# Performance work log

Measured on AMD Instinct MI355X. Metric: run time of the kernel, lower is better.

The kernel has to match this reference:

```python
import jax, jax.numpy as jnp
import numpy as np
import math

HIDDEN = 2048
N_HEADS = 16
HEAD_DIM = HIDDEN // N_HEADS
ROPE_BASE = 10000.0


def setup_inputs() -> dict:
    key = jax.random.key(0)
    ks = jax.random.split(key, 5)
    B, S = 2, 2048
    hidden_states = jax.random.normal(ks[0], (B, S, HIDDEN), dtype=jnp.float32)
    # additive causal mask (bsz, 1, q_len, kv_len)
    causal = jnp.tril(jnp.ones((S, S), dtype=bool))
    attention_mask = jnp.where(causal, 0.0, jnp.finfo(jnp.float32).min)[None, None].astype(jnp.float32)
    attention_mask = jnp.broadcast_to(attention_mask, (B, 1, S, S))
    position_ids = jnp.broadcast_to(jnp.arange(S, dtype=jnp.int32)[None], (B, S))
    scale = 1.0 / math.sqrt(HIDDEN)
    Wq = jax.random.normal(ks[1], (HIDDEN, HIDDEN), dtype=jnp.float32) * scale
    Wk = jax.random.normal(ks[2], (HIDDEN, HIDDEN), dtype=jnp.float32) * scale
    Wv = jax.random.normal(ks[3], (HIDDEN, HIDDEN), dtype=jnp.float32) * scale
    Wo = jax.random.normal(ks[4], (HIDDEN, HIDDEN), dtype=jnp.float32) * scale
    return {"hidden_states": hidden_states, "attention_mask": attention_mask,
            "position_ids": position_ids, "Wq": Wq, "Wk": Wk, "Wv": Wv, "Wo": Wo}


def _rotate_half(x):
    x1, x2 = jnp.split(x, 2, axis=-1)
    return jnp.concatenate([-x2, x1], axis=-1)


def _rope_cos_sin(position_ids, head_dim, dtype):
    inv_freq = 1.0 / (ROPE_BASE ** (jnp.arange(0, head_dim, 2, dtype=jnp.float32) / head_dim))
    freqs = position_ids.astype(jnp.float32)[..., None] * inv_freq  # [B, S, hd/2]
    emb = jnp.concatenate([freqs, freqs], axis=-1)                  # [B, S, hd]
    # unsqueeze head dim -> [B, 1, S, hd]
    return jnp.cos(emb)[:, None].astype(dtype), jnp.sin(emb)[:, None].astype(dtype)


def reference(hidden_states, attention_mask, position_ids, Wq, Wk, Wv, Wo):
    B, S, _ = hidden_states.shape
    H, D = N_HEADS, HEAD_DIM
    # projections (nn.Linear: x @ W.T); split heads -> [B, H, S, D]
    def proj(W):
        return jnp.einsum('bsh,oh->bso', hidden_states, W).reshape(B, S, H, D).transpose(0, 2, 1, 3)
    q, k, v = proj(Wq), proj(Wk), proj(Wv)
    cos, sin = _rope_cos_sin(position_ids, D, hidden_states.dtype)
    q = q * cos + _rotate_half(q) * sin
    k = k * cos + _rotate_half(k) * sin
    scores = jnp.einsum('bhqd,bhkd->bhqk', q, k) / math.sqrt(D)
    scores = scores + attention_mask
    probs = jax.nn.softmax(scores.astype(jnp.float32), axis=-1).astype(q.dtype)
    attn = jnp.einsum('bhqk,bhkd->bhqd', probs, v)
    attn = attn.transpose(0, 2, 1, 3).reshape(B, S, H * D)
    return jnp.einsum('bso,ho->bsh', attn, Wo)
```

## Files before the change

kernel.cpp:

```cpp
#include <hip/hip_runtime.h>
#include <cstdint>

typedef unsigned short u16t;
typedef float v4f __attribute__((ext_vector_type(4)));
typedef short v8s __attribute__((ext_vector_type(8)));

#define HIDDEN 2048
#define NHEAD 16
#define HDIM 128
#define SEQ 2048
#define BATCH 2
#define MROWS (BATCH * SEQ)

__device__ __forceinline__ float bf2f(u16t u) {
  return __builtin_bit_cast(float, (uint32_t)((uint32_t)u << 16));
}
__device__ __forceinline__ u16t f2bf(float f) {
  uint32_t u = __builtin_bit_cast(uint32_t, f);
  u += 0x7FFFu + ((u >> 16) & 1u);
  return (u16t)(u >> 16);
}
__device__ __forceinline__ ushort4 f2bf4(float4 v) {
  ushort4 r;
  r.x = f2bf(v.x); r.y = f2bf(v.y); r.z = f2bf(v.z); r.w = f2bf(v.w);
  return r;
}

__device__ __forceinline__ void gld_lds16(const u16t* g, u16t* l) {
  __builtin_amdgcn_global_load_lds(
      (const __attribute__((address_space(1))) uint32_t*)g,
      (__attribute__((address_space(3))) uint32_t*)l, 16, 0, 0);
}

__global__ __launch_bounds__(256) void cvt_bf16(const float* __restrict__ src,
                                                u16t* __restrict__ dst, int n8) {
  int i = blockIdx.x * 256 + threadIdx.x;
  if (i < n8) {
    float4 a = ((const float4*)src)[2 * i];
    float4 b = ((const float4*)src)[2 * i + 1];
    union { ushort4 h[2]; uint4 u; } pk;
    pk.h[0] = f2bf4(a);
    pk.h[1] = f2bf4(b);
    ((uint4*)dst)[i] = pk.u;
  }
}

__global__ __launch_bounds__(256) void cvt_bf16_w4(
    const float* __restrict__ s0, const float* __restrict__ s1,
    const float* __restrict__ s2, const float* __restrict__ s3,
    u16t* __restrict__ d0, u16t* __restrict__ d1,
    u16t* __restrict__ d2, u16t* __restrict__ d3) {
  int i = blockIdx.x * 256 + threadIdx.x;
  int sel = i >> 19;
  int j = i & 0x7FFFF;
  const float* src = (sel == 0) ? s0 : (sel == 1) ? s1 : (sel == 2) ? s2 : s3;
  u16t* dst = (sel == 0) ? d0 : (sel == 1) ? d1 : (sel == 2) ? d2 : d3;
  float4 a = ((const float4*)src)[2 * j];
  float4 b = ((const float4*)src)[2 * j + 1];
  union { ushort4 h[2]; uint4 u; } pk;
  pk.h[0] = f2bf4(a);
  pk.h[1] = f2bf4(b);
  ((uint4*)dst)[j] = pk.u;
}

template <int OUT>
__global__ __launch_bounds__(512) void gemm8p(const u16t* __restrict__ A,
                                              const u16t* __restrict__ B,
                                              void* __restrict__ Cp) {
  __shared__ u16t lds[73728];

  const int n0 = blockIdx.x * 128;
  const int m0 = blockIdx.y * 256;
  const int t = threadIdx.x;
  const int lane = t & 63;
  const int w = t >> 6;
  const int wm = w >> 2;
  const int wn = w & 3;
  const int l15 = lane & 15;
  const int quad = lane >> 4;
  const int l7 = l15 & 7;

  const int lrow = lane >> 3;
  const int lcol8 = ((lane & 7) ^ lrow) * 8;
  const u16t* Ag = A + (size_t)(m0 + w * 32 + lrow) * HIDDEN + lcol8;
  const u16t* Bg = B + (size_t)(n0 + w * 16 + lrow) * HIDDEN + lcol8;

  const int ca0 = (quad * 8) ^ (l7 * 8);
  const int ca1 = (32 + quad * 8) ^ (l7 * 8);

  v4f acc[8][2];
#pragma unroll
  for (int i = 0; i < 8; ++i)
#pragma unroll
    for (int j = 0; j < 2; ++j) acc[i][j] = (v4f){0.f, 0.f, 0.f, 0.f};

  const int KT = HIDDEN / 64;

#pragma unroll
  for (int tt = 0; tt < 2; ++tt) {
    const int kb = tt * 64;
#pragma unroll
    for (int j = 0; j < 4; ++j)
      gld_lds16(Ag + kb + j * 8 * HIDDEN,
                &lds[tt * 16384 + (w * 4 + j) * 512 + lane * 8]);
#pragma unroll
    for (int j = 0; j < 2; ++j)
      gld_lds16(Bg + kb + j * 8 * HIDDEN,
                &lds[49152 + tt * 8192 + (w * 2 + j) * 512 + lane * 8]);
  }
  asm volatile("s_waitcnt vmcnt(6)" ::: "memory");
  __builtin_amdgcn_s_barrier();

  int b = 0;
  for (int kt = 0; kt < KT; ++kt) {
    const int kb2 = kt * 64 + 128;
    const int b2 = (b >= 1) ? b - 1 : 2;
    const u16t* Asb = &lds[b * 16384];
    const u16t* Bsb = &lds[49152 + b * 8192];
    const bool pre = (kt + 2 < KT);

    v8s b0[2], b1[2];
#pragma unroll
    for (int j = 0; j < 2; ++j) {
      const u16t* p = Bsb + (wn * 32 + j * 16 + l15) * 64;
      b0[j] = *(const v8s*)(p + ca0);
      b1[j] = *(const v8s*)(p + ca1);
    }
    v8s a0[4], a1[4];
#pragma unroll
    for (int i = 0; i < 4; ++i) {
      const u16t* p = Asb + (wm * 128 + i * 16 + l15) * 64;
      a0[i] = *(const v8s*)(p + ca0);
      a1[i] = *(const v8s*)(p + ca1);
    }
    if (pre) {
      gld_lds16(Ag + kb2, &lds[b2 * 16384 + (w * 4 + 0) * 512 + lane * 8]);
      gld_lds16(Ag + kb2 + 8 * HIDDEN, &lds[b2 * 16384 + (w * 4 + 1) * 512 + lane * 8]);
      gld_lds16(Bg + kb2, &lds[49152 + b2 * 8192 + (w * 2 + 0) * 512 + lane * 8]);
    }
    __builtin_amdgcn_s_barrier();
    asm volatile("s_waitcnt lgkmcnt(0)" ::: "memory");
    __builtin_amdgcn_s_setprio(1);
#pragma unroll
    for (int i = 0; i < 4; ++i)
#pragma unroll
      for (int j = 0; j < 2; ++j) {
        acc[i][j] = __builtin_amdgcn_mfma_f32_16x16x32_bf16(a0[i], b0[j], acc[i][j], 0, 0, 0);
        acc[i][j] = __builtin_amdgcn_mfma_f32_16x16x32_bf16(a1[i], b1[j], acc[i][j], 0, 0, 0);
      }
    __builtin_amdgcn_s_setprio(0);
    __builtin_amdgcn_s_barrier();

#pragma unroll
    for (int i = 0; i < 4; ++i) {
      const u16t* p = Asb + (wm * 128 + 64 + i * 16 + l15) * 64;
      a0[i] = *(const v8s*)(p + ca0);
      a1[i] = *(const v8s*)(p + ca1);
    }
    if (pre) {
      gld_lds16(Ag + kb2 + 16 * HIDDEN, &lds[b2 * 16384 + (w * 4 + 2) * 512 + lane * 8]);
      gld_lds16(Ag + kb2 + 24 * HIDDEN, &lds[b2 * 16384 + (w * 4 + 3) * 512 + lane * 8]);
      gld_lds16(Bg + kb2 + 8 * HIDDEN, &lds[49152 + b2 * 8192 + (w * 2 + 1) * 512 + lane * 8]);
    }
    __builtin_amdgcn_s_barrier();
    asm volatile("s_waitcnt lgkmcnt(0)" ::: "memory");
    __builtin_amdgcn_s_setprio(1);
#pragma unroll
    for (int i = 0; i < 4; ++i)
#pragma unroll
      for (int j = 0; j < 2; ++j) {
        acc[4 + i][j] = __builtin_amdgcn_mfma_f32_16x16x32_bf16(a0[i], b0[j], acc[4 + i][j], 0, 0, 0);
        acc[4 + i][j] = __builtin_amdgcn_mfma_f32_16x16x32_bf16(a1[i], b1[j], acc[4 + i][j], 0, 0, 0);
      }
    __builtin_amdgcn_s_setprio(0);
    if (pre) {
      asm volatile("s_waitcnt vmcnt(6)" ::: "memory");
    } else if (kt + 1 < KT) {
      asm volatile("s_waitcnt vmcnt(0)" ::: "memory");
    }
    __builtin_amdgcn_s_barrier();
    b = (b == 2) ? 0 : b + 1;
  }

  if (OUT == 2) {
    u16t* Ct = (u16t*)lds;
    __syncthreads();
#pragma unroll
    for (int i = 0; i < 8; ++i)
#pragma unroll
      for (int j = 0; j < 2; ++j)
#pragma unroll
        for (int r = 0; r < 4; ++r)
          Ct[(wn * 32 + j * 16 + l15) * 264 + wm * 128 + i * 16 + quad * 4 + r] =
              f2bf(acc[i][j][r]);
    __syncthreads();
    u16t* VtOut = (u16t*)Cp;
#pragma unroll
    for (int it = 0; it < 8; ++it) {
      int idx = t + it * 512;
      int nl = idx >> 5;
      int mc = idx & 31;
      *(uint4*)&VtOut[(size_t)(n0 + nl) * MROWS + m0 + mc * 8] =
          *(const uint4*)&Ct[nl * 264 + mc * 8];
    }
  } else {
#pragma unroll
    for (int i = 0; i < 8; ++i) {
#pragma unroll
      for (int j = 0; j < 2; ++j) {
        int col = n0 + wn * 32 + j * 16 + l15;
#pragma unroll
        for (int r = 0; r < 4; ++r) {
          int row = m0 + wm * 128 + i * 16 + quad * 4 + r;
          if (OUT == 1)
            ((float*)Cp)[(size_t)row * HIDDEN + col] = acc[i][j][r];
          else
            ((u16t*)Cp)[(size_t)row * HIDDEN + col] = f2bf(acc[i][j][r]);
        }
      }
    }
  }
}

template <int OUT_F32>
__global__ __launch_bounds__(256) void gemm_a16(const u16t* __restrict__ A,
                                                const void* __restrict__ Bp,
                                                void* __restrict__ Cp) {
  __shared__ u16t As[128 * 32];
  __shared__ u16t Bs[128 * 32];

  const int n0 = blockIdx.x * 128;
  const int m0 = blockIdx.y * 128;
  const int t = threadIdx.x;
  const int lane = t & 63;
  const int w = t >> 6;
  const int wm = w & 1;
  const int wn = w >> 1;
  const int l15 = lane & 15;
  const int quad = lane >> 4;

  v4f acc[4][4];
#pragma unroll
  for (int i = 0; i < 4; ++i)
#pragma unroll
    for (int j = 0; j < 4; ++j) acc[i][j] = (v4f){0.f, 0.f, 0.f, 0.f};

  for (int kb = 0; kb < HIDDEN; kb += 32) {
#pragma unroll
    for (int j = 0; j < 2; ++j) {
      int idx = t + j * 256;
      int row = idx >> 2;
      int ch = (idx & 3) * 8;
      gld_lds16(&A[(size_t)(m0 + row) * HIDDEN + kb + ch], &As[idx * 8]);
    }
    {
      const float* B = (const float*)Bp;
#pragma unroll
      for (int j = 0; j < 4; ++j) {
        int idx = t + j * 256;
        int row = idx >> 3;
        int c4 = (idx & 7) * 4;
        float4 bv = *(const float4*)&B[(size_t)(n0 + row) * HIDDEN + kb + c4];
        *(ushort4*)&Bs[row * 32 + c4] = f2bf4(bv);
      }
    }
    __syncthreads();

    v8s af[4], bf[4];
#pragma unroll
    for (int mt = 0; mt < 4; ++mt)
      af[mt] = *(const v8s*)&As[(wm * 64 + mt * 16 + l15) * 32 + quad * 8];
#pragma unroll
    for (int nt = 0; nt < 4; ++nt)
      bf[nt] = *(const v8s*)&Bs[(wn * 64 + nt * 16 + l15) * 32 + quad * 8];

#pragma unroll
    for (int mt = 0; mt < 4; ++mt)
#pragma unroll
      for (int nt = 0; nt < 4; ++nt)
        acc[mt][nt] = __builtin_amdgcn_mfma_f32_16x16x32_bf16(af[mt], bf[nt], acc[mt][nt], 0, 0, 0);
    __syncthreads();
  }

#pragma unroll
  for (int mt = 0; mt < 4; ++mt) {
#pragma unroll
    for (int nt = 0; nt < 4; ++nt) {
      int col = n0 + wn * 64 + nt * 16 + l15;
#pragma unroll
      for (int r = 0; r < 4; ++r) {
        int row = m0 + wm * 64 + mt * 16 + quad * 4 + r;
        if (OUT_F32)
          ((float*)Cp)[(size_t)row * HIDDEN + col] = acc[mt][nt][r];
        else
          ((u16t*)Cp)[(size_t)row * HIDDEN + col] = f2bf(acc[mt][nt][r]);
      }
    }
  }
}

__global__ __launch_bounds__(256) void gemm_vt_f32(const u16t* __restrict__ A,
                                                   const void* __restrict__ Bp,
                                                   u16t* __restrict__ VtOut) {
  __shared__ u16t As[128 * 32];
  __shared__ u16t Bs[128 * 32];
  __shared__ u16t Ct[128 * 136];

  const int n0 = blockIdx.x * 128;
  const int m0 = blockIdx.y * 128;
  const int t = threadIdx.x;
  const int lane = t & 63;
  const int w = t >> 6;
  const int wm = w & 1;
  const int wn = w >> 1;
  const int l15 = lane & 15;
  const int quad = lane >> 4;

  v4f acc[4][4];
#pragma unroll
  for (int i = 0; i < 4; ++i)
#pragma unroll
    for (int j = 0; j < 4; ++j) acc[i][j] = (v4f){0.f, 0.f, 0.f, 0.f};

  for (int kb = 0; kb < HIDDEN; kb += 32) {
#pragma unroll
    for (int j = 0; j < 2; ++j) {
      int idx = t + j * 256;
      int row = idx >> 2;
      int ch = (idx & 3) * 8;
      gld_lds16(&A[(size_t)(m0 + row) * HIDDEN + kb + ch], &As[idx * 8]);
    }
    {
      const float* B = (const float*)Bp;
#pragma unroll
      for (int j = 0; j < 4; ++j) {
        int idx = t + j * 256;
        int row = idx >> 3;
        int c4 = (idx & 7) * 4;
        float4 bv = *(const float4*)&B[(size_t)(n0 + row) * HIDDEN + kb + c4];
        *(ushort4*)&Bs[row * 32 + c4] = f2bf4(bv);
      }
    }
    __syncthreads();

    v8s af[4], bf[4];
#pragma unroll
    for (int mt = 0; mt < 4; ++mt)
      af[mt] = *(const v8s*)&As[(wm * 64 + mt * 16 + l15) * 32 + quad * 8];
#pragma unroll
    for (int nt = 0; nt < 4; ++nt)
      bf[nt] = *(const v8s*)&Bs[(wn * 64 + nt * 16 + l15) * 32 + quad * 8];

#pragma unroll
    for (int mt = 0; mt < 4; ++mt)
#pragma unroll
      for (int nt = 0; nt < 4; ++nt)
        acc[mt][nt] = __builtin_amdgcn_mfma_f32_16x16x32_bf16(af[mt], bf[nt], acc[mt][nt], 0, 0, 0);
    __syncthreads();
  }

#pragma unroll
  for (int mt = 0; mt < 4; ++mt)
#pragma unroll
    for (int nt = 0; nt < 4; ++nt)
#pragma unroll
      for (int r = 0; r < 4; ++r)
        Ct[(wn * 64 + nt * 16 + l15) * 136 + (wm * 64 + mt * 16 + quad * 4 + r)] =
            f2bf(acc[mt][nt][r]);
  __syncthreads();

#pragma unroll
  for (int j = 0; j < 8; ++j) {
    int idx = t + j * 256;
    int nl = idx >> 4;
    int mc = idx & 15;
    *(uint4*)&VtOut[(size_t)(n0 + nl) * MROWS + m0 + mc * 8] =
        *(const uint4*)&Ct[nl * 136 + mc * 8];
  }
}

__global__ __launch_bounds__(256) void rope_k(u16t* __restrict__ q, u16t* __restrict__ k) {
  int idx = blockIdx.x * 256 + threadIdx.x;
  int i = idx & 63;
  int h = (idx >> 6) & (NHEAD - 1);
  int m = idx >> 10;
  int s = m & (SEQ - 1);
  float inv = __expf(-(float)i * 0.14391156831212787f);
  float th = (float)s * inv;
  float sn, cs;
  __sincosf(th, &sn, &cs);
  size_t base = (size_t)m * HIDDEN + h * HDIM + i;
  {
    float a = bf2f(q[base]), b = bf2f(q[base + 64]);
    q[base] = f2bf(a * cs - b * sn);
    q[base + 64] = f2bf(b * cs + a * sn);
  }
  {
    float a = bf2f(k[base]), b = bf2f(k[base + 64]);
    k[base] = f2bf(a * cs - b * sn);
    k[base + 64] = f2bf(b * cs + a * sn);
  }
}

__global__ __launch_bounds__(512) void flash2(const u16t* __restrict__ Q,
                                              const u16t* __restrict__ K,
                                              const u16t* __restrict__ Vt,
                                              u16t* __restrict__ O) {
  __shared__ u16t smem[40960];
  u16t* Ps = smem + 32768;

  const int a = blockIdx.x;
  const int bh = blockIdx.y;
  const int b = bh >> 4;
  const int h = bh & 15;
  const size_t rowb = (size_t)b * SEQ;
  const u16t* vtg = Vt + (size_t)h * HDIM * MROWS + (size_t)b * SEQ;

  const int t = threadIdx.x;
  const int lane = t & 63;
  const int w = t >> 6;
  const int l15 = lane & 15;
  const int quad = lane >> 4;
  const int l7 = l15 & 7;
  const float C2 = 0.12751743f;
  const float NEG = -3.0e38f;

  const int krow = t >> 4;
  const int kch = (t & 15) * 8;
  const int vrow = t >> 3;
  const int vch = (t & 7) * 8;
  const int kx = kch ^ ((krow & 7) * 8);
  const int vx = vch ^ ((vrow & 7) * 8);
  const u16t* Kgb = &K[(rowb + krow) * HIDDEN + h * HDIM + kch];
  const u16t* Vgb = vtg + (size_t)vrow * MROWS + vch;

  for (int half = 0; half < 2; ++half) {
    const int qt = half ? (15 - a) : a;
    const int q0 = qt * 128;
    const int nsteps = 2 * (qt + 1);

    uint4 ck0 = *(const uint4*)Kgb;
    uint4 ck1 = *(const uint4*)(Kgb + 32 * HIDDEN);
    uint4 cv0 = *(const uint4*)Vgb;
    uint4 cv1 = *(const uint4*)(Vgb + (size_t)64 * MROWS);

#pragma unroll
    for (int j = 0; j < 4; ++j) {
      int idx = t + j * 512;
      int row = idx >> 4;
      int ch = (idx & 15) * 8;
      *(uint4*)&smem[row * 136 + ch] =
          *(const uint4*)&Q[(rowb + q0 + row) * HIDDEN + h * HDIM + ch];
    }
    __syncthreads();
    v8s qf[4];
#pragma unroll
    for (int ks = 0; ks < 4; ++ks)
      qf[ks] = *(const v8s*)&smem[(w * 16 + l15) * 136 + ks * 32 + quad * 8];
    __syncthreads();

    float mi[4], li[4];
    v4f o[8];
#pragma unroll
    for (int r = 0; r < 4; ++r) { mi[r] = NEG; li[r] = 0.f; }
#pragma unroll
    for (int nt = 0; nt < 8; ++nt) o[nt] = (v4f){0.f, 0.f, 0.f, 0.f};

    for (int kt = 0; kt < nsteps; ++kt) {
      u16t* Kb = smem + (kt & 1) * 16384;
      u16t* Vb = Kb + 8192;
      *(uint4*)&Kb[krow * 128 + kx] = ck0;
      *(uint4*)&Kb[(krow + 32) * 128 + kx] = ck1;
      *(uint4*)&Vb[vrow * 64 + vx] = cv0;
      *(uint4*)&Vb[(vrow + 64) * 64 + vx] = cv1;
      if (kt + 1 < nsteps) {
        const int kv1 = (kt + 1) * 64;
        const u16t* kg = Kgb + (size_t)kv1 * HIDDEN;
        ck0 = *(const uint4*)kg;
        ck1 = *(const uint4*)(kg + 32 * HIDDEN);
        const u16t* vg = Vgb + kv1;
        cv0 = *(const uint4*)vg;
        cv1 = *(const uint4*)(vg + (size_t)64 * MROWS);
      }
      __syncthreads();

      const int kv0 = kt * 64;
      v4f sc[4];
#pragma unroll
      for (int nt = 0; nt < 4; ++nt) {
        sc[nt] = (v4f){0.f, 0.f, 0.f, 0.f};
#pragma unroll
        for (int ks = 0; ks < 4; ++ks) {
          v8s kf = *(const v8s*)&Kb[(nt * 16 + l15) * 128 +
                                    ((ks * 32 + quad * 8) ^ (l7 * 8))];
          sc[nt] = __builtin_amdgcn_mfma_f32_16x16x32_bf16(qf[ks], kf, sc[nt], 0, 0, 0);
        }
      }

      const bool mm = (kv0 + 64 > q0);
#pragma unroll
      for (int r = 0; r < 4; ++r) {
        float sv[4];
#pragma unroll
        for (int nt = 0; nt < 4; ++nt) sv[nt] = sc[nt][r];
        if (mm) {
          int row_g = q0 + w * 16 + quad * 4 + r;
#pragma unroll
          for (int nt = 0; nt < 4; ++nt)
            if (kv0 + nt * 16 + l15 > row_g) sv[nt] = NEG;
        }
        float rm = fmaxf(fmaxf(sv[0], sv[1]), fmaxf(sv[2], sv[3]));
#pragma unroll
        for (int off = 1; off < 16; off <<= 1) rm = fmaxf(rm, __shfl_xor(rm, off));
        float mn = fmaxf(mi[r], rm);
        float alpha = exp2f((mi[r] - mn) * C2);
        float ps = 0.f;
        u16t pb[4];
#pragma unroll
        for (int nt = 0; nt < 4; ++nt) {
          float p = exp2f((sv[nt] - mn) * C2);
          ps += p;
          pb[nt] = f2bf(p);
        }
#pragma unroll
        for (int off = 1; off < 16; off <<= 1) ps += __shfl_xor(ps, off);
        li[r] = li[r] * alpha + ps;
        mi[r] = mn;
#pragma unroll
        for (int nt = 0; nt < 8; ++nt) o[nt][r] *= alpha;
        int rowp = w * 16 + quad * 4 + r;
        int psw = (rowp & 7) * 8;
#pragma unroll
        for (int nt = 0; nt < 4; ++nt)
          Ps[rowp * 64 + ((nt * 16 + l15) ^ psw)] = pb[nt];
      }

#pragma unroll
      for (int ks = 0; ks < 2; ++ks) {
        v8s pf = *(const v8s*)&Ps[(w * 16 + l15) * 64 +
                                  ((ks * 32 + quad * 8) ^ (l7 * 8))];
#pragma unroll
        for (int nt = 0; nt < 8; ++nt) {
          v8s vf = *(const v8s*)&Vb[(nt * 16 + l15) * 64 +
                                    ((ks * 32 + quad * 8) ^ (l7 * 8))];
          o[nt] = __builtin_amdgcn_mfma_f32_16x16x32_bf16(pf, vf, o[nt], 0, 0, 0);
        }
      }
    }

#pragma unroll
    for (int r = 0; r < 4; ++r) {
      float inv = 1.0f / li[r];
      size_t row = rowb + q0 + w * 16 + quad * 4 + r;
#pragma unroll
      for (int nt = 0; nt < 8; ++nt)
        O[row * HIDDEN + h * HDIM + nt * 16 + l15] = f2bf(o[nt][r] * inv);
    }
    __syncthreads();
  }
}

extern "C" void kernel_launch(void* const* d_in, const int* in_sizes, int n_in,
                              void* d_out, int out_size, void* d_ws, size_t ws_size,
                              hipStream_t stream) {
  const float* X = (const float*)d_in[0];
  const float* Wq = (const float*)d_in[3];
  const float* Wk = (const float*)d_in[4];
  const float* Wv = (const float*)d_in[5];
  const float* Wo = (const float*)d_in[6];
  float* out = (float*)d_out;

  char* wsb = (char*)d_ws;
  const size_t MB = 1024 * 1024;
  u16t* xb = (u16t*)(wsb + 0 * MB);
  u16t* q = (u16t*)(wsb + 16 * MB);
  u16t* k = (u16t*)(wsb + 32 * MB);
  u16t* vt = (u16t*)(wsb + 48 * MB);
  u16t* a = xb;

  dim3 blk(256);
  dim3 fg(8, BATCH * NHEAD);
  const int XN8 = MROWS * HIDDEN / 8;
  const int WN8 = HIDDEN * HIDDEN / 8;

  cvt_bf16<<<(XN8 + 255) / 256, blk, 0, stream>>>(X, xb, XN8);

  if (ws_size >= 96 * MB) {
    u16t* wqb = (u16t*)(wsb + 64 * MB);
    u16t* wkb = (u16t*)(wsb + 72 * MB);
    u16t* wvb = (u16t*)(wsb + 80 * MB);
    u16t* wob = (u16t*)(wsb + 88 * MB);
    cvt_bf16_w4<<<(4 * WN8) / 256, blk, 0, stream>>>(Wq, Wk, Wv, Wo, wqb, wkb, wvb, wob);

    dim3 g8(HIDDEN / 128, MROWS / 256);
    gemm8p<0><<<g8, dim3(512), 0, stream>>>(xb, wqb, q);
    gemm8p<0><<<g8, dim3(512), 0, stream>>>(xb, wkb, k);
    gemm8p<2><<<g8, dim3(512), 0, stream>>>(xb, wvb, vt);
    rope_k<<<(MROWS * NHEAD * 64) / 256, blk, 0, stream>>>(q, k);
    flash2<<<fg, dim3(512), 0, stream>>>(q, k, vt, a);
    gemm8p<1><<<g8, dim3(512), 0, stream>>>(a, wob, out);
  } else {
    dim3 gg(HIDDEN / 128, MROWS / 128);
    gemm_a16<0><<<gg, blk, 0, stream>>>(xb, Wq, q);
    gemm_a16<0><<<gg, blk, 0, stream>>>(xb, Wk, k);
    gemm_vt_f32<<<gg, blk, 0, stream>>>(xb, Wv, vt);
    rope_k<<<(MROWS * NHEAD * 64) / 256, blk, 0, stream>>>(q, k);
    flash2<<<fg, dim3(512), 0, stream>>>(q, k, vt, a);
    gemm_a16<1><<<gg, blk, 0, stream>>>(a, Wo, out);
  }
}
```

Baseline: 424.3 us.

## Fuse Q/K/V projections into one 256x256-tile GEMM with block swizzle

Replaces three separate Q, K and V projection GEMM launches with a single launch of 384 blocks. The launch treats the contiguous bf16 Wq/Wk/Wv buffers as one 6144-row weight and routes each tile's output to q, k or the transposed V. The tile grows from 256x128 to 256x256, the K step shrinks from 64 to 32, and a block-id swizzle is added for L2 locality. The output projection reuses the same kernel with only 128 blocks, which cuts launch overhead but may leave many CUs idle.

```diff
diff --git a/kernel.cpp b/kernel.cpp
--- a/kernel.cpp
+++ b/kernel.cpp
@@ -63,14 +63,24 @@
   ((uint4*)dst)[j] = pk.u;
 }
 
-template <int OUT>
-__global__ __launch_bounds__(512) void gemm8p(const u16t* __restrict__ A,
-                                              const u16t* __restrict__ B,
-                                              void* __restrict__ Cp) {
-  __shared__ u16t lds[73728];
-
-  const int n0 = blockIdx.x * 128;
-  const int m0 = blockIdx.y * 256;
+template <int MODE>
+__global__ __launch_bounds__(512) void gemm_fused(const u16t* __restrict__ A,
+                                                  const u16t* __restrict__ B,
+                                                  u16t* __restrict__ qo,
+                                                  u16t* __restrict__ ko,
+                                                  u16t* __restrict__ vto,
+                                                  float* __restrict__ fo) {
+  __shared__ u16t lds[49152];
+
+  const int NX = (MODE == 0) ? 24 : 8;
+  const int CPX = (MODE == 0) ? 48 : 16;
+  const int id = blockIdx.x;
+  const int swz = (id & 7) * CPX + (id >> 3);
+  const int tx = swz % NX;
+  const int ty = swz / NX;
+  const int n0 = tx * 256;
+  const int m0 = ty * 256;
+
   const int t = threadIdx.x;
   const int lane = t & 63;
   const int w = t >> 6;
@@ -78,65 +88,52 @@
   const int wn = w & 3;
   const int l15 = lane & 15;
   const int quad = lane >> 4;
-  const int l7 = l15 & 7;
-
-  const int lrow = lane >> 3;
-  const int lcol8 = ((lane & 7) ^ lrow) * 8;
-  const u16t* Ag = A + (size_t)(m0 + w * 32 + lrow) * HIDDEN + lcol8;
-  const u16t* Bg = B + (size_t)(n0 + w * 16 + lrow) * HIDDEN + lcol8;
-
-  const int ca0 = (quad * 8) ^ (l7 * 8);
-  const int ca1 = (32 + quad * 8) ^ (l7 * 8);
-
-  v4f acc[8][2];
+
+  const int srow = t >> 2;
+  const int sc8 = ((t & 3) ^ ((t >> 3) & 3)) * 8;
+  const u16t* Ag = A + (size_t)(m0 + srow) * HIDDEN + sc8;
+  const u16t* Bg = B + (size_t)(n0 + srow) * HIDDEN + sc8;
+
+  const int pcol = (quad ^ ((l15 >> 1) & 3)) * 8;
+
+  v4f acc[8][4];
 #pragma unroll
   for (int i = 0; i < 8; ++i)
 #pragma unroll
-    for (int j = 0; j < 2; ++j) acc[i][j] = (v4f){0.f, 0.f, 0.f, 0.f};
-
-  const int KT = HIDDEN / 64;
+    for (int j = 0; j < 4; ++j) acc[i][j] = (v4f){0.f, 0.f, 0.f, 0.f};
+
+  const int KT = HIDDEN / 32;
 
 #pragma unroll
   for (int tt = 0; tt < 2; ++tt) {
-    const int kb = tt * 64;
-#pragma unroll
-    for (int j = 0; j < 4; ++j)
-      gld_lds16(Ag + kb + j * 8 * HIDDEN,
-                &lds[tt * 16384 + (w * 4 + j) * 512 + lane * 8]);
-#pragma unroll
-    for (int j = 0; j < 2; ++j)
-      gld_lds16(Bg + kb + j * 8 * HIDDEN,
-                &lds[49152 + tt * 8192 + (w * 2 + j) * 512 + lane * 8]);
-  }
-  asm volatile("s_waitcnt vmcnt(6)" ::: "memory");
+    const int kb = tt * 32;
+    gld_lds16(Ag + kb, &lds[tt * 8192 + t * 8]);
+    gld_lds16(Ag + kb + 128 * HIDDEN, &lds[tt * 8192 + 4096 + t * 8]);
+    gld_lds16(Bg + kb, &lds[24576 + tt * 8192 + t * 8]);
+    gld_lds16(Bg + kb + 128 * HIDDEN, &lds[24576 + tt * 8192 + 4096 + t * 8]);
+  }
+  asm volatile("s_waitcnt vmcnt(4)" ::: "memory");
   __builtin_amdgcn_s_barrier();
 
   int b = 0;
   for (int kt = 0; kt < KT; ++kt) {
-    const int kb2 = kt * 64 + 128;
+    const int kb2 = kt * 32 + 64;
     const int b2 = (b >= 1) ? b - 1 : 2;
-    const u16t* Asb = &lds[b * 16384];
-    const u16t* Bsb = &lds[49152 + b * 8192];
+    const u16t* Asb = &lds[b * 8192];
+    const u16t* Bsb = &lds[24576 + b * 8192];
     const bool pre = (kt + 2 < KT);
 
-    v8s b0[2], b1[2];
-#pragma unroll
-    for (int j = 0; j < 2; ++j) {
-      const u16t* p = Bsb + (wn * 32 + j * 16 + l15) * 64;
-      b0[j] = *(const v8s*)(p + ca0);
-      b1[j] = *(const v8s*)(p + ca1);
-    }
-    v8s a0[4], a1[4];
-#pragma unroll
-    for (int i = 0; i < 4; ++i) {
-      const u16t* p = Asb + (wm * 128 + i * 16 + l15) * 64;
-      a0[i] = *(const v8s*)(p + ca0);
-      a1[i] = *(const v8s*)(p + ca1);
-    }
+    v8s bfr[4];
+#pragma unroll
+    for (int j = 0; j < 4; ++j)
+      bfr[j] = *(const v8s*)&Bsb[(wn * 64 + j * 16 + l15) * 32 + pcol];
+    v8s af[4];
+#pragma unroll
+    for (int i = 0; i < 4; ++i)
+      af[i] = *(const v8s*)&Asb[(wm * 128 + i * 16 + l15) * 32 + pcol];
     if (pre) {
-      gld_lds16(Ag + kb2, &lds[b2 * 16384 + (w * 4 + 0) * 512 + lane * 8]);
-      gld_lds16(Ag + kb2 + 8 * HIDDEN, &lds[b2 * 16384 + (w * 4 + 1) * 512 + lane * 8]);
-      gld_lds16(Bg + kb2, &lds[49152 + b2 * 8192 + (w * 2 + 0) * 512 + lane * 8]);
+      gld_lds16(Ag + kb2, &lds[b2 * 8192 + t * 8]);
+      gld_lds16(Bg + kb2, &lds[24576 + b2 * 8192 + t * 8]);
     }
     __builtin_amdgcn_s_barrier();
     asm volatile("s_waitcnt lgkmcnt(0)" ::: "memory");
@@ -144,23 +141,17 @@
 #pragma unroll
     for (int i = 0; i < 4; ++i)
 #pragma unroll
-      for (int j = 0; j < 2; ++j) {
-        acc[i][j] = __builtin_amdgcn_mfma_f32_16x16x32_bf16(a0[i], b0[j], acc[i][j], 0, 0, 0);
-        acc[i][j] = __builtin_amdgcn_mfma_f32_16x16x32_bf16(a1[i], b1[j], acc[i][j], 0, 0, 0);
-      }
+      for (int j = 0; j < 4; ++j)
+        acc[i][j] = __builtin_amdgcn_mfma_f32_16x16x32_bf16(af[i], bfr[j], acc[i][j], 0, 0, 0);
     __builtin_amdgcn_s_setprio(0);
     __builtin_amdgcn_s_barrier();
 
 #pragma unroll
-    for (int i = 0; i < 4; ++i) {
-      const u16t* p = Asb + (wm * 128 + 64 + i * 16 + l15) * 64;
-      a0[i] = *(const v8s*)(p + ca0);
-      a1[i] = *(const v8s*)(p + ca1);
-    }
+    for (int i = 0; i < 4; ++i)
+      af[i] = *(const v8s*)&Asb[(wm * 128 + 64 + i * 16 + l15) * 32 + pcol];
     if (pre) {
-      gld_lds16(Ag + kb2 + 16 * HIDDEN, &lds[b2 * 16384 + (w * 4 + 2) * 512 + lane * 8]);
-      gld_lds16(Ag + kb2 + 24 * HIDDEN, &lds[b2 * 16384 + (w * 4 + 3) * 512 + lane * 8]);
-      gld_lds16(Bg + kb2 + 8 * HIDDEN, &lds[49152 + b2 * 8192 + (w * 2 + 1) * 512 + lane * 8]);
+      gld_lds16(Ag + kb2 + 128 * HIDDEN, &lds[b2 * 8192 + 4096 + t * 8]);
+      gld_lds16(Bg + kb2 + 128 * HIDDEN, &lds[24576 + b2 * 8192 + 4096 + t * 8]);
     }
     __builtin_amdgcn_s_barrier();
     asm volatile("s_waitcnt lgkmcnt(0)" ::: "memory");
@@ -168,13 +159,11 @@
 #pragma unroll
     for (int i = 0; i < 4; ++i)
 #pragma unroll
-      for (int j = 0; j < 2; ++j) {
-        acc[4 + i][j] = __builtin_amdgcn_mfma_f32_16x16x32_bf16(a0[i], b0[j], acc[4 + i][j], 0, 0, 0);
-        acc[4 + i][j] = __builtin_amdgcn_mfma_f32_16x16x32_bf16(a1[i], b1[j], acc[4 + i][j], 0, 0, 0);
-      }
+      for (int j = 0; j < 4; ++j)
+        acc[4 + i][j] = __builtin_amdgcn_mfma_f32_16x16x32_bf16(af[i], bfr[j], acc[4 + i][j], 0, 0, 0);
     __builtin_amdgcn_s_setprio(0);
     if (pre) {
-      asm volatile("s_waitcnt vmcnt(6)" ::: "memory");
+      asm volatile("s_waitcnt vmcnt(4)" ::: "memory");
     } else if (kt + 1 < KT) {
       asm volatile("s_waitcnt vmcnt(0)" ::: "memory");
     }
@@ -182,41 +171,58 @@
     b = (b == 2) ? 0 : b + 1;
   }
 
-  if (OUT == 2) {
-    u16t* Ct = (u16t*)lds;
-    __syncthreads();
-#pragma unroll
-    for (int i = 0; i < 8; ++i)
-#pragma unroll
-      for (int j = 0; j < 2; ++j)
-#pragma unroll
-        for (int r = 0; r < 4; ++r)
-          Ct[(wn * 32 + j * 16 + l15) * 264 + wm * 128 + i * 16 + quad * 4 + r] =
-              f2bf(acc[i][j][r]);
-    __syncthreads();
-    u16t* VtOut = (u16t*)Cp;
-#pragma unroll
-    for (int it = 0; it < 8; ++it) {
-      int idx = t + it * 512;
-      int nl = idx >> 5;
-      int mc = idx & 31;
-      *(uint4*)&VtOut[(size_t)(n0 + nl) * MROWS + m0 + mc * 8] =
-          *(const uint4*)&Ct[nl * 264 + mc * 8];
-    }
-  } else {
+  if (MODE == 1) {
 #pragma unroll
     for (int i = 0; i < 8; ++i) {
 #pragma unroll
-      for (int j = 0; j < 2; ++j) {
-        int col = n0 + wn * 32 + j * 16 + l15;
+      for (int j = 0; j < 4; ++j) {
+        int col = n0 + wn * 64 + j * 16 + l15;
 #pragma unroll
         for (int r = 0; r < 4; ++r) {
           int row = m0 + wm * 128 + i * 16 + quad * 4 + r;
-          if (OUT == 1)
-            ((float*)Cp)[(size_t)row * HIDDEN + col] = acc[i][j][r];
-          else
-            ((u16t*)Cp)[(size_t)row * HIDDEN + col] = f2bf(acc[i][j][r]);
+          fo[(size_t)row * HIDDEN + col] = acc[i][j][r];
         }
+      }
+    }
+  } else if (tx < 16) {
+    u16t* dst = (tx < 8) ? qo : ko;
+    const int cb = n0 & 2047;
+#pragma unroll
+    for (int i = 0; i < 8; ++i) {
+#pragma unroll
+      for (int j = 0; j < 4; ++j) {
+        int col = cb + wn * 64 + j * 16 + l15;
+#pragma unroll
+        for (int r = 0; r < 4; ++r) {
+          int row = m0 + wm * 128 + i * 16 + quad * 4 + r;
+          dst[(size_t)row * HIDDEN + col] = f2bf(acc[i][j][r]);
+        }
+      }
+    }
+  } else {
+    const int nv0 = n0 - 4096;
+    u16t* Ct = (u16t*)lds;
+#pragma unroll
+    for (int h = 0; h < 2; ++h) {
+      __syncthreads();
+      if ((wn >> 1) == h) {
+#pragma unroll
+        for (int i = 0; i < 8; ++i)
+#pragma unroll
+          for (int j = 0; j < 4; ++j)
+#pragma unroll
+            for (int r = 0; r < 4; ++r)
+              Ct[((wn & 1) * 64 + j * 16 + l15) * 264 +
+                 wm * 128 + i * 16 + quad * 4 + r] = f2bf(acc[i][j][r]);
+      }
+      __syncthreads();
+#pragma unroll
+      for (int it = 0; it < 8; ++it) {
+        int idx = t + it * 512;
+        int nl = idx >> 5;
+        int mc = idx & 31;
+        *(uint4*)&vto[(size_t)(nv0 + h * 128 + nl) * MROWS + m0 + mc * 8] =
+            *(const uint4*)&Ct[nl * 264 + mc * 8];
       }
     }
   }
@@ -592,13 +598,10 @@
     u16t* wob = (u16t*)(wsb + 88 * MB);
     cvt_bf16_w4<<<(4 * WN8) / 256, blk, 0, stream>>>(Wq, Wk, Wv, Wo, wqb, wkb, wvb, wob);
 
-    dim3 g8(HIDDEN / 128, MROWS / 256);
-    gemm8p<0><<<g8, dim3(512), 0, stream>>>(xb, wqb, q);
-    gemm8p<0><<<g8, dim3(512), 0, stream>>>(xb, wkb, k);
-    gemm8p<2><<<g8, dim3(512), 0, stream>>>(xb, wvb, vt);
+    gemm_fused<0><<<dim3(384), dim3(512), 0, stream>>>(xb, wqb, q, k, vt, nullptr);
     rope_k<<<(MROWS * NHEAD * 64) / 256, blk, 0, stream>>>(q, k);
     flash2<<<fg, dim3(512), 0, stream>>>(q, k, vt, a);
-    gemm8p<1><<<g8, dim3(512), 0, stream>>>(a, wob, out);
+    gemm_fused<1><<<dim3(128), dim3(512), 0, stream>>>(a, wob, nullptr, nullptr, nullptr, out);
   } else {
     dim3 gg(HIDDEN / 128, MROWS / 128);
     gemm_a16<0><<<gg, blk, 0, stream>>>(xb, Wq, q);
```

Result: slower. 440.3 us (+3.8%).
